# Performance work log

Hardware: AMD Instinct MI355X
Metric: run time of the kernel (lower is better)

## Reference

```python
import jax, jax.numpy as jnp
import numpy as np

B, S, IN_DIM, H, D = 2, 2048, 1024, 16, 64

def setup_inputs() -> dict:
    key = jax.random.key(0)
    ks = jax.random.split(key, 8)
    Q = jax.random.normal(ks[0], (B, S, IN_DIM), dtype=jnp.float32)
    K = jax.random.normal(ks[1], (B, S, IN_DIM), dtype=jnp.float32)
    V = jax.random.normal(ks[2], (B, S, IN_DIM), dtype=jnp.float32)
    # True = masked position (matches torch masked_fill_ semantics)
    attn_mask = jax.random.bernoulli(ks[3], 0.1, (B, S, S))
    scale = 1.0 / np.sqrt(IN_DIM)
    Wq = jax.random.normal(ks[4], (IN_DIM, H * D), dtype=jnp.float32) * scale
    Wk = jax.random.normal(ks[5], (IN_DIM, H * D), dtype=jnp.float32) * scale
    Wv = jax.random.normal(ks[6], (IN_DIM, H * D), dtype=jnp.float32) * scale
    Wo = jax.random.normal(ks[7], (H * D, IN_DIM), dtype=jnp.float32) * scale
    return {"Q": Q, "K": K, "V": V, "attn_mask": attn_mask,
            "Wq": Wq, "Wk": Wk, "Wv": Wv, "Wo": Wo}

def reference(Q, K, V, attn_mask, Wq, Wk, Wv, Wo):
    b, s, _ = Q.shape
    # Projections -> [B, H, S, D]
    q = (Q @ Wq).reshape(b, s, H, D).transpose(0, 2, 1, 3)
    k = (K @ Wk).reshape(b, s, H, D).transpose(0, 2, 1, 3)
    v = (V @ Wv).reshape(b, s, H, D).transpose(0, 2, 1, 3)
    scores = jnp.einsum('bhqd,bhkd->bhqk', q, k) / np.sqrt(D)
    scores = jnp.where(attn_mask[:, None, :, :], jnp.float32(-1e9), scores)
    attn = jax.nn.softmax(scores, axis=-1)
    ctx = jnp.einsum('bhqk,bhkd->bhqd', attn, v)  # [B, H, S, D]
    ctx = ctx.transpose(0, 2, 1, 3).reshape(b, s, H * D)
    return ctx @ Wo + Q
```

## Files before the change

### kernel.cpp

```cpp
#include <hip/hip_runtime.h>
#include <hip/hip_bf16.h>


#define BB   2
#define SS   2048
#define IND  1024
#define HH   16
#define DD   64
#define MM_ELEMS 524288

typedef __attribute__((ext_vector_type(8))) short  s8b;
typedef __attribute__((ext_vector_type(4))) short  s4b;
typedef __attribute__((ext_vector_type(4))) float  f32x4;

static __device__ __forceinline__ short f2b(float x) {
    return __builtin_bit_cast(short, __float2bfloat16(x));
}

#define GLD16(g, l)                                                             \
    __builtin_amdgcn_global_load_lds(                                           \
        (const __attribute__((address_space(1))) unsigned int*)(g),             \
        (__attribute__((address_space(3))) unsigned int*)(l), 16, 0, 0)

__global__ __launch_bounds__(256) void wconv(const float* __restrict__ w0,
                                             const float* __restrict__ w1,
                                             const float* __restrict__ w2,
                                             const float* __restrict__ w3,
                                             short* __restrict__ out) {
    const int z = blockIdx.z;
    const float* src = (z == 0) ? w0 : (z == 1) ? w1 : (z == 2) ? w2 : w3;
    const float wscale = (z == 0) ? 0.125f : 1.0f;
    short* dst = out + (size_t)z * IND * IND;
    __shared__ __attribute__((aligned(16))) short ls[64][72];
    const int t  = threadIdx.x;
    const int k0 = blockIdx.y * 64;
    const int n0 = blockIdx.x * 64;
#pragma unroll
    for (int p = 0; p < 4; ++p) {
        int ch = t + p * 256;
        int r  = ch >> 4;
        int c4 = ch & 15;
        float4 v = *reinterpret_cast<const float4*>(&src[(size_t)(k0 + r) * IND + n0 + c4 * 4]);
        ls[r][c4 * 4 + 0] = f2b(v.x * wscale);
        ls[r][c4 * 4 + 1] = f2b(v.y * wscale);
        ls[r][c4 * 4 + 2] = f2b(v.z * wscale);
        ls[r][c4 * 4 + 3] = f2b(v.w * wscale);
    }
    __syncthreads();
#pragma unroll
    for (int p = 0; p < 2; ++p) {
        int ch = t + p * 256;
        int nr = ch >> 3;
        int kg = ch & 7;
        s8b o;
#pragma unroll
        for (int j = 0; j < 8; ++j) o[j] = ls[kg * 8 + j][nr];
        *reinterpret_cast<s8b*>(&dst[(size_t)(n0 + nr) * IND + k0 + kg * 8]) = o;
    }
}

__global__ __launch_bounds__(256) void maskpack(const unsigned char* __restrict__ mask,
                                                unsigned long long* __restrict__ bits) {
    __shared__ int s_flag;
    const int t = threadIdx.x;
    if (t == 0) s_flag = 0;
    __syncthreads();
    {
        int bad = 0;
#pragma unroll
        for (int i = 0; i < 16; ++i) {
            int idx = t * 16 + i;
            if ((idx & 3) && mask[idx]) bad = 1;
        }
        if (bad) s_flag = 1;
    }
    __syncthreads();
    const bool isI32 = (s_flag == 0);

    const int lane = t & 63;
    const size_t nwords = (size_t)BB * SS * SS / 64;
    size_t w = (size_t)blockIdx.x * 4 + (t >> 6);
    const size_t stride = (size_t)gridDim.x * 4;
    if (isI32) {
        const unsigned* m4 = (const unsigned*)mask;
        for (; w < nwords; w += stride) {
            unsigned long long bal = __ballot(m4[w * 64 + lane] != 0);
            if (lane == 0) bits[w] = bal;
        }
    } else {
        for (; w < nwords; w += stride) {
            unsigned long long bal = __ballot(mask[w * 64 + lane] != 0);
            if (lane == 0) bits[w] = bal;
        }
    }
}

__global__ __launch_bounds__(256) void cvt3(const float* __restrict__ q,
                                            const float* __restrict__ k,
                                            const float* __restrict__ v,
                                            short* __restrict__ o) {
    const size_t nchunk = (size_t)3 * MM_ELEMS;
    size_t i = (size_t)blockIdx.x * 256 + threadIdx.x;
    const size_t stride = (size_t)gridDim.x * 256;
    for (; i < nchunk; i += stride) {
        size_t base = i * 8;
        int z = (int)(base >> 22);
        size_t off = base & 4194303u;
        const float* src = (z == 0) ? q : (z == 1) ? k : v;
        float4 a = *reinterpret_cast<const float4*>(&src[off]);
        float4 b = *reinterpret_cast<const float4*>(&src[off + 4]);
        s8b w;
        w[0] = f2b(a.x); w[1] = f2b(a.y); w[2] = f2b(a.z); w[3] = f2b(a.w);
        w[4] = f2b(b.x); w[5] = f2b(b.y); w[6] = f2b(b.z); w[7] = f2b(b.w);
        *reinterpret_cast<s8b*>(&o[base]) = w;
    }
}

__global__ __launch_bounds__(256) void gemm_qkv(const short* __restrict__ abf,
                                                const short* __restrict__ wt,
                                                short* __restrict__ qb,
                                                short* __restrict__ kb,
                                                short* __restrict__ vt) {
    __shared__ __attribute__((aligned(16))) short lsA[128 * 32];
    __shared__ __attribute__((aligned(16))) short lsB[128 * 32];
    const int z = blockIdx.z;
    const short* A  = abf + (size_t)z * 4194304;
    const short* Bt = wt + (size_t)z * IND * IND;

    const int t    = threadIdx.x;
    const int lane = t & 63;
    const int wv   = t >> 6;
    const int wr   = wv >> 1, wc = wv & 1;
    const int m0   = blockIdx.y * 128, n0 = blockIdx.x * 128;
    const int lr   = lane & 15;
    const int lg   = lane >> 4;
    const int rs   = lane >> 2;
    const int cs   = lane & 3;

    f32x4 acc[4][4] = {};

    for (int k0 = 0; k0 < IND; k0 += 32) {
        __syncthreads();
        GLD16(&A [(size_t)(m0 + wv * 16      + rs) * IND + k0 + cs * 8], &lsA[ wv      * 512]);
        GLD16(&A [(size_t)(m0 + (wv+4) * 16  + rs) * IND + k0 + cs * 8], &lsA[(wv + 4) * 512]);
        GLD16(&Bt[(size_t)(n0 + wv * 16      + rs) * IND + k0 + cs * 8], &lsB[ wv      * 512]);
        GLD16(&Bt[(size_t)(n0 + (wv+4) * 16  + rs) * IND + k0 + cs * 8], &lsB[(wv + 4) * 512]);
        __syncthreads();

        s8b af[4], bfr[4];
#pragma unroll
        for (int mi = 0; mi < 4; ++mi)
            af[mi] = *reinterpret_cast<const s8b*>(&lsA[(wr * 64 + mi * 16 + lr) * 32 + lg * 8]);
#pragma unroll
        for (int nj = 0; nj < 4; ++nj)
            bfr[nj] = *reinterpret_cast<const s8b*>(&lsB[(wc * 64 + nj * 16 + lr) * 32 + lg * 8]);
#pragma unroll
        for (int mi = 0; mi < 4; ++mi)
#pragma unroll
            for (int nj = 0; nj < 4; ++nj)
                acc[mi][nj] = __builtin_amdgcn_mfma_f32_16x16x32_bf16(af[mi], bfr[nj], acc[mi][nj], 0, 0, 0);
    }

#pragma unroll
    for (int mi = 0; mi < 4; ++mi) {
#pragma unroll
        for (int nj = 0; nj < 4; ++nj) {
            const int mbase = m0 + wr * 64 + mi * 16 + lg * 4;
            const int n     = n0 + wc * 64 + nj * 16 + lr;
            if (z < 2) {
                short* o = z ? kb : qb;
                const int h = n >> 6, d = n & 63;
#pragma unroll
                for (int i = 0; i < 4; ++i) {
                    int m = mbase + i;
                    int b = m >> 11, s = m & 2047;
                    o[((size_t)(b * HH + h) * SS + s) * DD + d] = f2b(acc[mi][nj][i]);
                }
            } else {
                const int b = mbase >> 11, sbase = mbase & 2047;
                const int h = n >> 6, d = n & 63;
                s4b w;
#pragma unroll
                for (int i = 0; i < 4; ++i) w[i] = f2b(acc[mi][nj][i]);
                *reinterpret_cast<s4b*>(&vt[((size_t)(b * HH + h) * DD + d) * SS + sbase]) = w;
            }
        }
    }
}

__global__ __launch_bounds__(256) void attn(const short* __restrict__ qb,
                                            const short* __restrict__ kb,
                                            const short* __restrict__ vt,
                                            const unsigned* __restrict__ mbw,
                                            short* __restrict__ ctx) {
    __shared__ __attribute__((aligned(16))) short lsK[64 * 64];
    __shared__ __attribute__((aligned(16))) short lsV[64 * 64];
    __shared__ __attribute__((aligned(16))) short lsP[4][16 * 72];

    const int t    = threadIdx.x;
    const int lane = t & 63;
    const int wv   = t >> 6;
    const int bh   = blockIdx.y;
    const int b    = bh >> 4, h = bh & 15;
    const int q0   = blockIdx.x * 64 + wv * 16;
    const int lr   = lane & 15;
    const int lg   = lane >> 4;

    const unsigned sel0 = 1u << lr;
    const unsigned sel1 = sel0 << 16;
    const uint2* mrp = (const uint2*)(mbw + (size_t)(b * SS + q0 + lg * 4) * (SS / 32));

    const int rk = lane >> 3;
    const int ck = (lane & 7) ^ rk;
    const short* kbase = kb + (size_t)bh * SS * DD;
    const short* vbase = vt + (size_t)bh * DD * SS;

    s8b aq[2];
#pragma unroll
    for (int ks = 0; ks < 2; ++ks)
        aq[ks] = *reinterpret_cast<const s8b*>(&qb[((size_t)bh * SS + q0 + lr) * DD + ks * 32 + lg * 8]);

    s8b ones;
#pragma unroll
    for (int j = 0; j < 8; ++j) ones[j] = (short)0x3F80;

    f32x4 o[4] = {};
    float lrow[4] = {0.f, 0.f, 0.f, 0.f};

#pragma unroll
    for (int c = 0; c < 2; ++c) {
        int chunk = wv + c * 4;
        int row = chunk * 8 + rk;
        GLD16(&kbase[(size_t)row * DD + ck * 8], &lsK[chunk * 512]);
        GLD16(&vbase[(size_t)row * SS + ck * 8], &lsV[chunk * 512]);
    }

    for (int kk0 = 0; kk0 < SS; kk0 += 64) {
        uint2 mw[4];
#pragma unroll
        for (int i = 0; i < 4; ++i) mw[i] = mrp[i * 32 + (kk0 >> 6)];

        __syncthreads();

        f32x4 sc[4];
#pragma unroll
        for (int nj = 0; nj < 4; ++nj) {
            const int R  = nj * 16 + lr;
            const int sw = R & 7;
            s8b bk0 = *reinterpret_cast<const s8b*>(&lsK[R * 64 + ((lg ^ sw) << 3)]);
            s8b bk1 = *reinterpret_cast<const s8b*>(&lsK[R * 64 + (((lg ^ 4) ^ sw) << 3)]);
            f32x4 zz = {};
            zz     = __builtin_amdgcn_mfma_f32_16x16x32_bf16(aq[0], bk0, zz, 0, 0, 0);
            sc[nj] = __builtin_amdgcn_mfma_f32_16x16x32_bf16(aq[1], bk1, zz, 0, 0, 0);
        }

#pragma unroll
        for (int nj = 0; nj < 4; ++nj) {
            const unsigned slm = (nj & 1) ? sel1 : sel0;
#pragma unroll
            for (int i = 0; i < 4; ++i) {
                unsigned w = (nj < 2) ? mw[i].x : mw[i].y;
                float e = __expf(sc[nj][i]);
                float p = (w & slm) ? 0.f : e;
                lsP[wv][(lg * 4 + i) * 72 + nj * 16 + lr] = f2b(p);
            }
        }

        s8b pa[2];
#pragma unroll
        for (int ks = 0; ks < 2; ++ks)
            pa[ks] = *reinterpret_cast<const s8b*>(&lsP[wv][lr * 72 + ks * 32 + lg * 8]);

        f32x4 rs = {};
        rs = __builtin_amdgcn_mfma_f32_16x16x32_bf16(pa[0], ones, rs, 0, 0, 0);
        rs = __builtin_amdgcn_mfma_f32_16x16x32_bf16(pa[1], ones, rs, 0, 0, 0);

#pragma unroll
        for (int nj = 0; nj < 4; ++nj) {
            const int R  = nj * 16 + lr;
            const int sw = R & 7;
            s8b bv0 = *reinterpret_cast<const s8b*>(&lsV[R * 64 + ((lg ^ sw) << 3)]);
            s8b bv1 = *reinterpret_cast<const s8b*>(&lsV[R * 64 + (((lg ^ 4) ^ sw) << 3)]);
            o[nj] = __builtin_amdgcn_mfma_f32_16x16x32_bf16(pa[0], bv0, o[nj], 0, 0, 0);
            o[nj] = __builtin_amdgcn_mfma_f32_16x16x32_bf16(pa[1], bv1, o[nj], 0, 0, 0);
        }
#pragma unroll
        for (int i = 0; i < 4; ++i) lrow[i] += rs[i];

        __syncthreads();

        if (kk0 + 64 < SS) {
#pragma unroll
            for (int c = 0; c < 2; ++c) {
                int chunk = wv + c * 4;
                int row = chunk * 8 + rk;
                GLD16(&kbase[(size_t)(kk0 + 64 + row) * DD + ck * 8], &lsK[chunk * 512]);
                GLD16(&vbase[(size_t)row * SS + kk0 + 64 + ck * 8], &lsV[chunk * 512]);
            }
        }
    }

    float inv[4];
#pragma unroll
    for (int i = 0; i < 4; ++i) inv[i] = 1.0f / lrow[i];
#pragma unroll
    for (int nj = 0; nj < 4; ++nj)
#pragma unroll
        for (int i = 0; i < 4; ++i) {
            int q = q0 + lg * 4 + i;
            ctx[((size_t)(b * SS + q)) * (HH * DD) + h * DD + nj * 16 + lr] = f2b(o[nj][i] * inv[i]);
        }
}

__global__ __launch_bounds__(256) void gemm_out(const short* __restrict__ Actx,
                                                const short* __restrict__ Bt,
                                                const float* __restrict__ resid,
                                                float* __restrict__ outp) {
    __shared__ __attribute__((aligned(16))) short lsA[64 * 32];
    __shared__ __attribute__((aligned(16))) short lsB[128 * 32];
    const int t    = threadIdx.x;
    const int lane = t & 63;
    const int wv   = t >> 6;
    const int wr   = wv >> 1, wc = wv & 1;
    const int m0   = blockIdx.y * 64, n0 = blockIdx.x * 128;
    const int lr   = lane & 15;
    const int lg   = lane >> 4;
    const int rs   = lane >> 2;
    const int cs   = lane & 3;

    f32x4 acc[2][4] = {};

    for (int k0 = 0; k0 < IND; k0 += 32) {
        __syncthreads();
        GLD16(&Actx[(size_t)(m0 + wv * 16     + rs) * IND + k0 + cs * 8], &lsA[ wv      * 512]);
        GLD16(&Bt  [(size_t)(n0 + wv * 16     + rs) * IND + k0 + cs * 8], &lsB[ wv      * 512]);
        GLD16(&Bt  [(size_t)(n0 + (wv+4) * 16 + rs) * IND + k0 + cs * 8], &lsB[(wv + 4) * 512]);
        __syncthreads();

        s8b af[2], bfr[4];
#pragma unroll
        for (int mi = 0; mi < 2; ++mi)
            af[mi] = *reinterpret_cast<const s8b*>(&lsA[(wr * 32 + mi * 16 + lr) * 32 + lg * 8]);
#pragma unroll
        for (int nj = 0; nj < 4; ++nj)
            bfr[nj] = *reinterpret_cast<const s8b*>(&lsB[(wc * 64 + nj * 16 + lr) * 32 + lg * 8]);
#pragma unroll
        for (int mi = 0; mi < 2; ++mi)
#pragma unroll
            for (int nj = 0; nj < 4; ++nj)
                acc[mi][nj] = __builtin_amdgcn_mfma_f32_16x16x32_bf16(af[mi], bfr[nj], acc[mi][nj], 0, 0, 0);
    }

#pragma unroll
    for (int mi = 0; mi < 2; ++mi)
#pragma unroll
        for (int nj = 0; nj < 4; ++nj) {
            const int mbase = m0 + wr * 32 + mi * 16 + lg * 4;
            const int n     = n0 + wc * 64 + nj * 16 + lr;
#pragma unroll
            for (int i = 0; i < 4; ++i) {
                int m = mbase + i;
                outp[(size_t)m * IND + n] = acc[mi][nj][i] + resid[(size_t)m * IND + n];
            }
        }
}

extern "C" void kernel_launch(void* const* d_in, const int* in_sizes, int n_in,
                              void* d_out, int out_size, void* d_ws, size_t ws_size,
                              hipStream_t stream) {
    const float* Qin = (const float*)d_in[0];
    const float* Kin = (const float*)d_in[1];
    const float* Vin = (const float*)d_in[2];
    const unsigned char* mask = (const unsigned char*)d_in[3];
    const float* Wq = (const float*)d_in[4];
    const float* Wk = (const float*)d_in[5];
    const float* Wv = (const float*)d_in[6];
    const float* Wo = (const float*)d_in[7];

    char* ws = (char*)d_ws;
    const size_t WSZ = (size_t)IND * IND;
    short* wt  = (short*)ws;
    short* qb  = (short*)(ws + 8ull  * 1024 * 1024);
    short* kb  = (short*)(ws + 16ull * 1024 * 1024);
    short* vt  = (short*)(ws + 24ull * 1024 * 1024);
    unsigned long long* mbits = (unsigned long long*)(ws + 32ull * 1024 * 1024);
    short* abf = (short*)(ws + 36ull * 1024 * 1024);
    short* ctx = (short*)(ws + 36ull * 1024 * 1024);

    wconv   <<<dim3(16, 16, 4), 256, 0, stream>>>(Wq, Wk, Wv, Wo, wt);
    maskpack<<<512, 256, 0, stream>>>(mask, mbits);
    cvt3    <<<2048, 256, 0, stream>>>(Qin, Kin, Vin, abf);
    gemm_qkv<<<dim3(8, 32, 3), 256, 0, stream>>>(abf, wt, qb, kb, vt);
    attn    <<<dim3(SS / 64, BB * HH), 256, 0, stream>>>(qb, kb, vt, (const unsigned*)mbits, ctx);
    gemm_out<<<dim3(8, 64), 256, 0, stream>>>(ctx, wt + 3 * WSZ, Qin, (float*)d_out);
}
```

Baseline: 293.3 us.

## Double K-tile depth with XOR-swizzled LDS in GEMMs, register-prefetch K/V in attention

```diff
diff --git a/kernel.cpp b/kernel.cpp
--- a/kernel.cpp
+++ b/kernel.cpp
@@ -121,8 +121,8 @@
                                                 short* __restrict__ qb,
                                                 short* __restrict__ kb,
                                                 short* __restrict__ vt) {
-    __shared__ __attribute__((aligned(16))) short lsA[128 * 32];
-    __shared__ __attribute__((aligned(16))) short lsB[128 * 32];
+    __shared__ __attribute__((aligned(16))) short lsA[128 * 64];
+    __shared__ __attribute__((aligned(16))) short lsB[128 * 64];
     const int z = blockIdx.z;
     const short* A  = abf + (size_t)z * 4194304;
     const short* Bt = wt + (size_t)z * IND * IND;
@@ -134,31 +134,41 @@
     const int m0   = blockIdx.y * 128, n0 = blockIdx.x * 128;
     const int lr   = lane & 15;
     const int lg   = lane >> 4;
-    const int rs   = lane >> 2;
-    const int cs   = lane & 3;
+    const int rk8  = lane >> 3;
+    const int gs   = (lane & 7) ^ rk8;
 
     f32x4 acc[4][4] = {};
 
-    for (int k0 = 0; k0 < IND; k0 += 32) {
-        __syncthreads();
-        GLD16(&A [(size_t)(m0 + wv * 16      + rs) * IND + k0 + cs * 8], &lsA[ wv      * 512]);
-        GLD16(&A [(size_t)(m0 + (wv+4) * 16  + rs) * IND + k0 + cs * 8], &lsA[(wv + 4) * 512]);
-        GLD16(&Bt[(size_t)(n0 + wv * 16      + rs) * IND + k0 + cs * 8], &lsB[ wv      * 512]);
-        GLD16(&Bt[(size_t)(n0 + (wv+4) * 16  + rs) * IND + k0 + cs * 8], &lsB[(wv + 4) * 512]);
-        __syncthreads();
-
-        s8b af[4], bfr[4];
-#pragma unroll
-        for (int mi = 0; mi < 4; ++mi)
-            af[mi] = *reinterpret_cast<const s8b*>(&lsA[(wr * 64 + mi * 16 + lr) * 32 + lg * 8]);
-#pragma unroll
-        for (int nj = 0; nj < 4; ++nj)
-            bfr[nj] = *reinterpret_cast<const s8b*>(&lsB[(wc * 64 + nj * 16 + lr) * 32 + lg * 8]);
-#pragma unroll
-        for (int mi = 0; mi < 4; ++mi)
-#pragma unroll
-            for (int nj = 0; nj < 4; ++nj)
-                acc[mi][nj] = __builtin_amdgcn_mfma_f32_16x16x32_bf16(af[mi], bfr[nj], acc[mi][nj], 0, 0, 0);
+    for (int k0 = 0; k0 < IND; k0 += 64) {
+        __syncthreads();
+#pragma unroll
+        for (int c = 0; c < 4; ++c) {
+            int chunk = wv * 4 + c;
+            int row = chunk * 8 + rk8;
+            GLD16(&A [(size_t)(m0 + row) * IND + k0 + gs * 8], &lsA[chunk * 512]);
+            GLD16(&Bt[(size_t)(n0 + row) * IND + k0 + gs * 8], &lsB[chunk * 512]);
+        }
+        __syncthreads();
+
+#pragma unroll
+        for (int ks = 0; ks < 2; ++ks) {
+            s8b af[4], bfr[4];
+#pragma unroll
+            for (int mi = 0; mi < 4; ++mi) {
+                int row = wr * 64 + mi * 16 + lr;
+                af[mi] = *reinterpret_cast<const s8b*>(&lsA[row * 64 + (((ks * 4 + lg) ^ (row & 7)) << 3)]);
+            }
+#pragma unroll
+            for (int nj = 0; nj < 4; ++nj) {
+                int row = wc * 64 + nj * 16 + lr;
+                bfr[nj] = *reinterpret_cast<const s8b*>(&lsB[row * 64 + (((ks * 4 + lg) ^ (row & 7)) << 3)]);
+            }
+#pragma unroll
+            for (int mi = 0; mi < 4; ++mi)
+#pragma unroll
+                for (int nj = 0; nj < 4; ++nj)
+                    acc[mi][nj] = __builtin_amdgcn_mfma_f32_16x16x32_bf16(af[mi], bfr[nj], acc[mi][nj], 0, 0, 0);
+        }
     }
 
 #pragma unroll
@@ -235,12 +245,24 @@
         GLD16(&vbase[(size_t)row * SS + ck * 8], &lsV[chunk * 512]);
     }
 
+    s8b kreg[2], vreg[2];
     for (int kk0 = 0; kk0 < SS; kk0 += 64) {
         uint2 mw[4];
 #pragma unroll
         for (int i = 0; i < 4; ++i) mw[i] = mrp[i * 32 + (kk0 >> 6)];
 
         __syncthreads();
+
+        const bool pf = (kk0 + 64 < SS);
+        if (pf) {
+#pragma unroll
+            for (int c = 0; c < 2; ++c) {
+                int chunk = wv + c * 4;
+                int row = chunk * 8 + rk;
+                kreg[c] = *reinterpret_cast<const s8b*>(&kbase[(size_t)(kk0 + 64 + row) * DD + ck * 8]);
+                vreg[c] = *reinterpret_cast<const s8b*>(&vbase[(size_t)row * SS + kk0 + 64 + ck * 8]);
+            }
+        }
 
         f32x4 sc[4];
 #pragma unroll
@@ -289,13 +311,12 @@
 
         __syncthreads();
 
-        if (kk0 + 64 < SS) {
+        if (pf) {
 #pragma unroll
             for (int c = 0; c < 2; ++c) {
                 int chunk = wv + c * 4;
-                int row = chunk * 8 + rk;
-                GLD16(&kbase[(size_t)(kk0 + 64 + row) * DD + ck * 8], &lsK[chunk * 512]);
-                GLD16(&vbase[(size_t)row * SS + kk0 + 64 + ck * 8], &lsV[chunk * 512]);
+                *reinterpret_cast<s8b*>(&lsK[chunk * 512 + lane * 8]) = kreg[c];
+                *reinterpret_cast<s8b*>(&lsV[chunk * 512 + lane * 8]) = vreg[c];
             }
         }
     }
@@ -316,8 +337,8 @@
                                                 const short* __restrict__ Bt,
                                                 const float* __restrict__ resid,
                                                 float* __restrict__ outp) {
-    __shared__ __attribute__((aligned(16))) short lsA[64 * 32];
-    __shared__ __attribute__((aligned(16))) short lsB[128 * 32];
+    __shared__ __attribute__((aligned(16))) short lsA[64 * 64];
+    __shared__ __attribute__((aligned(16))) short lsB[128 * 64];
     const int t    = threadIdx.x;
     const int lane = t & 63;
     const int wv   = t >> 6;
@@ -325,30 +346,46 @@
     const int m0   = blockIdx.y * 64, n0 = blockIdx.x * 128;
     const int lr   = lane & 15;
     const int lg   = lane >> 4;
-    const int rs   = lane >> 2;
-    const int cs   = lane & 3;
+    const int rk8  = lane >> 3;
+    const int gs   = (lane & 7) ^ rk8;
 
     f32x4 acc[2][4] = {};
 
-    for (int k0 = 0; k0 < IND; k0 += 32) {
-        __syncthreads();
-        GLD16(&Actx[(size_t)(m0 + wv * 16     + rs) * IND + k0 + cs * 8], &lsA[ wv      * 512]);
-        GLD16(&Bt  [(size_t)(n0 + wv * 16     + rs) * IND + k0 + cs * 8], &lsB[ wv      * 512]);
-        GLD16(&Bt  [(size_t)(n0 + (wv+4) * 16 + rs) * IND + k0 + cs * 8], &lsB[(wv + 4) * 512]);
-        __syncthreads();
-
-        s8b af[2], bfr[4];
-#pragma unroll
-        for (int mi = 0; mi < 2; ++mi)
-            af[mi] = *reinterpret_cast<const s8b*>(&lsA[(wr * 32 + mi * 16 + lr) * 32 + lg * 8]);
-#pragma unroll
-        for (int nj = 0; nj < 4; ++nj)
-            bfr[nj] = *reinterpret_cast<const s8b*>(&lsB[(wc * 64 + nj * 16 + lr) * 32 + lg * 8]);
-#pragma unroll
-        for (int mi = 0; mi < 2; ++mi)
-#pragma unroll
-            for (int nj = 0; nj < 4; ++nj)
-                acc[mi][nj] = __builtin_amdgcn_mfma_f32_16x16x32_bf16(af[mi], bfr[nj], acc[mi][nj], 0, 0, 0);
+    for (int k0 = 0; k0 < IND; k0 += 64) {
+        __syncthreads();
+#pragma unroll
+        for (int c = 0; c < 2; ++c) {
+            int chunk = wv * 2 + c;
+            int row = chunk * 8 + rk8;
+            GLD16(&Actx[(size_t)(m0 + row) * IND + k0 + gs * 8], &lsA[chunk * 512]);
+        }
+#pragma unroll
+        for (int c = 0; c < 4; ++c) {
+            int chunk = wv * 4 + c;
+            int row = chunk * 8 + rk8;
+            GLD16(&Bt[(size_t)(n0 + row) * IND + k0 + gs * 8], &lsB[chunk * 512]);
+        }
+        __syncthreads();
+
+#pragma unroll
+        for (int ks = 0; ks < 2; ++ks) {
+            s8b af[2], bfr[4];
+#pragma unroll
+            for (int mi = 0; mi < 2; ++mi) {
+                int row = wr * 32 + mi * 16 + lr;
+                af[mi] = *reinterpret_cast<const s8b*>(&lsA[row * 64 + (((ks * 4 + lg) ^ (row & 7)) << 3)]);
+            }
+#pragma unroll
+            for (int nj = 0; nj < 4; ++nj) {
+                int row = wc * 64 + nj * 16 + lr;
+                bfr[nj] = *reinterpret_cast<const s8b*>(&lsB[row * 64 + (((ks * 4 + lg) ^ (row & 7)) << 3)]);
+            }
+#pragma unroll
+            for (int mi = 0; mi < 2; ++mi)
+#pragma unroll
+                for (int nj = 0; nj < 4; ++nj)
+                    acc[mi][nj] = __builtin_amdgcn_mfma_f32_16x16x32_bf16(af[mi], bfr[nj], acc[mi][nj], 0, 0, 0);
+        }
     }
 
 #pragma unroll
```

Measured after the change: 303.2 us. 3.4% more time.
